# Kernel tuning notes

Measured on AMD Instinct MI355X. Metric: run time of the kernel, lower is better.

Reference implementation:

```python
import jax, jax.numpy as jnp
import numpy as np

NUM_CLASSES = 21
THRESH = 0.5
NEGPOS = 3
VAR0, VAR1 = 0.1, 0.2
FEAT = 19
N_ANCH = 9
B = 256
NUM_OBJS = 12
P = FEAT * FEAT * N_ANCH  # 3249


def make_priors():
    # 19x19 grid, 3 scales x 3 aspect ratios (1, 2, 1/2) -> 9 anchors/cell, center form
    cxy = (np.arange(FEAT, dtype=np.float32) + 0.5) / FEAT
    cx, cy = np.meshgrid(cxy, cxy, indexing='ij')  # [19,19]
    scales = np.array([0.1, 0.2, 0.35], dtype=np.float32)
    ratios = np.array([1.0, 2.0, 0.5], dtype=np.float32)
    w = (scales[:, None] * np.sqrt(ratios)[None, :]).reshape(-1)  # [9]
    h = (scales[:, None] / np.sqrt(ratios)[None, :]).reshape(-1)
    cx = np.broadcast_to(cx[:, :, None], (FEAT, FEAT, N_ANCH))
    cy = np.broadcast_to(cy[:, :, None], (FEAT, FEAT, N_ANCH))
    w = np.broadcast_to(w[None, None, :], (FEAT, FEAT, N_ANCH))
    h = np.broadcast_to(h[None, None, :], (FEAT, FEAT, N_ANCH))
    pri = np.stack([cx, cy, w, h], axis=-1).reshape(-1, 4)
    return jnp.asarray(np.clip(pri, 1e-3, 1.0))


def setup_inputs() -> dict:
    key = jax.random.key(0)
    k1, k2, k3, k4, k5 = jax.random.split(key, 5)
    loc_data = jax.random.normal(k1, (B, P, 4), dtype=jnp.float32)
    conf_data = jax.random.normal(k2, (B, P, NUM_CLASSES), dtype=jnp.float32)
    priors = make_priors()
    xy = jax.random.uniform(k3, (B, NUM_OBJS, 2), minval=0.05, maxval=0.65)
    wh = jax.random.uniform(k4, (B, NUM_OBJS, 2), minval=0.05, maxval=0.30)
    labels = jax.random.randint(k5, (B, NUM_OBJS), 0, NUM_CLASSES - 1).astype(jnp.float32)
    targets = jnp.concatenate([xy, xy + wh, labels[..., None]], axis=-1)  # [B,O,5]
    return {"loc_data": loc_data, "conf_data": conf_data, "priors": priors, "targets": targets}


def point_form(boxes):  # (cx,cy,w,h) -> (x1,y1,x2,y2)
    return jnp.concatenate([boxes[:, :2] - boxes[:, 2:] / 2,
                            boxes[:, :2] + boxes[:, 2:] / 2], axis=1)


def jaccard(a, b):  # a: [n,4], b: [m,4] point form -> [n,m]
    lt = jnp.maximum(a[:, None, :2], b[None, :, :2])
    rb = jnp.minimum(a[:, None, 2:], b[None, :, 2:])
    inter = jnp.prod(jnp.clip(rb - lt, 0.0, None), axis=-1)
    area_a = jnp.prod(a[:, 2:] - a[:, :2], axis=-1)
    area_b = jnp.prod(b[:, 2:] - b[:, :2], axis=-1)
    return inter / (area_a[:, None] + area_b[None, :] - inter)


def encode(matched, priors):  # matched point-form [P,4], priors center-form [P,4]
    g_cxcy = ((matched[:, :2] + matched[:, 2:]) / 2 - priors[:, :2]) / (VAR0 * priors[:, 2:])
    g_wh = jnp.log((matched[:, 2:] - matched[:, :2]) / priors[:, 2:]) / VAR1
    return jnp.concatenate([g_cxcy, g_wh], axis=1)


def match_one(truths, labels, priors, priors_pt):
    overlaps = jaccard(truths, priors_pt)          # [O,P]
    best_prior_idx = jnp.argmax(overlaps, axis=1)  # [O]
    best_truth_ov = jnp.max(overlaps, axis=0)      # [P]
    best_truth_idx = jnp.argmax(overlaps, axis=0)  # [P]
    best_truth_ov = best_truth_ov.at[best_prior_idx].set(2.0)
    best_truth_idx = best_truth_idx.at[best_prior_idx].set(jnp.arange(truths.shape[0]))
    matches = truths[best_truth_idx]               # [P,4]
    conf = labels[best_truth_idx] + 1
    conf = jnp.where(best_truth_ov < THRESH, 0, conf)
    return encode(matches, priors), conf


def reference(loc_data, conf_data, priors, targets):
    truths = targets[:, :, :4]
    labels = targets[:, :, 4].astype(jnp.int32)
    priors_pt = point_form(priors)
    loc_t, conf_t = jax.vmap(lambda t, l: match_one(t, l, priors, priors_pt))(truths, labels)
    loc_t = jax.lax.stop_gradient(loc_t)
    conf_t = jax.lax.stop_gradient(conf_t)

    pos = conf_t > 0                                               # [B,P]
    # smooth L1 (sum) over matched priors
    d = loc_data - loc_t
    ad = jnp.abs(d)
    sl1 = jnp.where(ad < 1.0, 0.5 * d * d, ad - 0.5)
    loss_l = jnp.sum(sl1 * pos[..., None].astype(sl1.dtype))

    # per-prior CE = logsumexp - logit[target]
    lse = jax.nn.logsumexp(conf_data, axis=-1)                     # [B,P]
    gathered = jnp.take_along_axis(conf_data, conf_t[..., None], axis=2)[..., 0]
    ce = lse - gathered                                            # [B,P]

    # hard negative mining: double argsort rank of neg losses
    loss_c_mine = jnp.where(pos, 0.0, ce)
    loss_idx = jnp.argsort(-loss_c_mine, axis=1)
    idx_rank = jnp.argsort(loss_idx, axis=1)
    num_pos = jnp.sum(pos, axis=1, keepdims=True)                  # [B,1]
    num_neg = jnp.minimum(NEGPOS * num_pos, P - 1)
    neg = idx_rank < num_neg

    sel = pos | neg
    loss_c = jnp.sum(jnp.where(sel, ce, 0.0))

    have_centerloss = jnp.max(sel.reshape(B, FEAT, FEAT, N_ANCH), axis=3).reshape(-1)
    conf_t_featuremap = jnp.max(conf_t.reshape(B, FEAT, FEAT, N_ANCH), axis=3).reshape(-1)

    N = jnp.sum(num_pos).astype(loc_data.dtype)
    return loss_l / N, loss_c / N, conf_t_featuremap, have_centerloss
```

## Files before the change

### kernel.cpp

```cpp
#include <hip/hip_runtime.h>
#include <math.h>

#pragma clang fp contract(off)

#define BB      256
#define PP      3249
#define NCLS    21
#define NOBJ    12
#define CELLS   361
#define THRESH_ 0.5f


__global__ __launch_bounds__(1024) void match_kernel(
    const float* __restrict__ loc,
    const float* __restrict__ priors, const float* __restrict__ targets,
    int* __restrict__ conf_t,
    int* __restrict__ numpos, double* __restrict__ lossl)
{
    const int b = blockIdx.x, tid = threadIdx.x;
    const int lane = tid & 63, wid = tid >> 6;
    __shared__ float s_tx1[NOBJ], s_ty1[NOBJ], s_tx2[NOBJ], s_ty2[NOBJ];
    __shared__ float s_area_t[NOBJ];
    __shared__ int   s_label[NOBJ];
    __shared__ float s_bov[PP];
    __shared__ short s_bidx[PP];
    __shared__ int   s_bpi[NOBJ];
    __shared__ float s_wov[NOBJ][16];
    __shared__ int   s_widx[NOBJ][16];
    __shared__ double s_pl[16];
    __shared__ int    s_pn[16];

    if (tid < NOBJ) {
        const float* t = targets + ((size_t)b * NOBJ + tid) * 5;
        float x1 = t[0], y1 = t[1], x2 = t[2], y2 = t[3];
        s_tx1[tid] = x1; s_ty1[tid] = y1; s_tx2[tid] = x2; s_ty2[tid] = y2;
        s_label[tid] = (int)t[4];
        s_area_t[tid] = (x2 - x1) * (y2 - y1);
    }
    __syncthreads();

    float l_bov[NOBJ];
    int   l_bidx[NOBJ];
#pragma unroll
    for (int j = 0; j < NOBJ; ++j) { l_bov[j] = -1.0f; l_bidx[j] = 0x7FFFFFFF; }

    for (int p = tid; p < PP; p += 1024) {
        float cx = priors[4*p+0], cy = priors[4*p+1], w = priors[4*p+2], h = priors[4*p+3];
        float px1 = cx - w / 2.0f, py1 = cy - h / 2.0f;
        float px2 = cx + w / 2.0f, py2 = cy + h / 2.0f;
        float area_p = (px2 - px1) * (py2 - py1);
        float bov = -1.0f; int bidx = 0;
#pragma unroll
        for (int j = 0; j < NOBJ; ++j) {
            float ltx = fmaxf(s_tx1[j], px1);
            float lty = fmaxf(s_ty1[j], py1);
            float rbx = fminf(s_tx2[j], px2);
            float rby = fminf(s_ty2[j], py2);
            float iw = fmaxf(rbx - ltx, 0.0f);
            float ih = fmaxf(rby - lty, 0.0f);
            float inter = iw * ih;
            float iou = inter / ((s_area_t[j] + area_p) - inter);
            if (iou > bov) { bov = iou; bidx = j; }
            if (iou > l_bov[j]) { l_bov[j] = iou; l_bidx[j] = p; }
        }
        s_bov[p] = bov;
        s_bidx[p] = (short)bidx;
    }

#pragma unroll
    for (int j = 0; j < NOBJ; ++j) {
        float ov = l_bov[j]; int ix = l_bidx[j];
#pragma unroll
        for (int off = 32; off > 0; off >>= 1) {
            float ov2 = __shfl_xor(ov, off);
            int   ix2 = __shfl_xor(ix, off);
            if (ov2 > ov || (ov2 == ov && ix2 < ix)) { ov = ov2; ix = ix2; }
        }
        if (lane == 0) { s_wov[j][wid] = ov; s_widx[j][wid] = ix; }
    }
    __syncthreads();

    if (tid < NOBJ) {
        float ov = s_wov[tid][0]; int ix = s_widx[tid][0];
#pragma unroll
        for (int w2 = 1; w2 < 16; ++w2) {
            float ov2 = s_wov[tid][w2]; int ix2 = s_widx[tid][w2];
            if (ov2 > ov || (ov2 == ov && ix2 < ix)) { ov = ov2; ix = ix2; }
        }
        s_bpi[tid] = ix;
    }
    __syncthreads();

    int my_pos = 0;
    double my_lossl = 0.0;
    for (int p = tid; p < PP; p += 1024) {
        int jov = -1;
#pragma unroll
        for (int j = 0; j < NOBJ; ++j) if (s_bpi[j] == p) jov = j;
        int idx; float ov;
        if (jov >= 0) { idx = jov; ov = 2.0f; }
        else          { idx = (int)s_bidx[p]; ov = s_bov[p]; }
        int c = (ov < THRESH_) ? 0 : (s_label[idx] + 1);
        conf_t[(size_t)b * PP + p] = c;

        if (c > 0) {
            ++my_pos;
            float cx = priors[4*p+0], cy = priors[4*p+1], w = priors[4*p+2], h = priors[4*p+3];
            float m0 = s_tx1[idx], m1 = s_ty1[idx], m2 = s_tx2[idx], m3 = s_ty2[idx];
            float g0 = ((m0 + m2) / 2.0f - cx) / (0.1f * w);
            float g1 = ((m1 + m3) / 2.0f - cy) / (0.1f * h);
            float g2 = logf((m2 - m0) / w) / 0.2f;
            float g3 = logf((m3 - m1) / h) / 0.2f;
            const float* ld = loc + ((size_t)b * PP + p) * 4;
            float d0 = ld[0] - g0, d1 = ld[1] - g1, d2 = ld[2] - g2, d3 = ld[3] - g3;
            float a0 = fabsf(d0), a1 = fabsf(d1), a2 = fabsf(d2), a3 = fabsf(d3);
            my_lossl += (double)((a0 < 1.0f) ? 0.5f * d0 * d0 : a0 - 0.5f);
            my_lossl += (double)((a1 < 1.0f) ? 0.5f * d1 * d1 : a1 - 0.5f);
            my_lossl += (double)((a2 < 1.0f) ? 0.5f * d2 * d2 : a2 - 0.5f);
            my_lossl += (double)((a3 < 1.0f) ? 0.5f * d3 * d3 : a3 - 0.5f);
        }
    }
#pragma unroll
    for (int off = 32; off > 0; off >>= 1) {
        my_lossl += __shfl_down(my_lossl, off);
        my_pos   += __shfl_down(my_pos, off);
    }
    if (lane == 0) { s_pl[wid] = my_lossl; s_pn[wid] = my_pos; }
    __syncthreads();
    if (tid == 0) {
        double L = 0.0; int n = 0;
#pragma unroll
        for (int w2 = 0; w2 < 16; ++w2) { L += s_pl[w2]; n += s_pn[w2]; }
        lossl[b] = L; numpos[b] = n;
    }
}

__global__ __launch_bounds__(256) void ce_kernel(
    const float* __restrict__ conf, const int* __restrict__ conf_t,
    float* __restrict__ ce_out)
{
    __shared__ float s_row[256 * NCLS];
    const int tid = threadIdx.x;
    const size_t base = (size_t)blockIdx.x * 256;
    const float4* src = (const float4*)(conf + base * NCLS);
    float4* dst = (float4*)s_row;
#pragma unroll
    for (int i = tid; i < 1344; i += 256) dst[i] = src[i];
    __syncthreads();

    const float* cd = s_row + tid * NCLS;
    float m = cd[0];
#pragma unroll
    for (int k = 1; k < NCLS; ++k) m = fmaxf(m, cd[k]);
    float s = 0.0f;
#pragma unroll
    for (int k = 0; k < NCLS; ++k) s += expf(cd[k] - m);
    float lse = logf(s) + m;
    const size_t r = base + tid;
    int c = conf_t[r];
    ce_out[r] = lse - cd[c];
}

__global__ __launch_bounds__(1024) void mine_kernel(
    const int* __restrict__ conf_t, const float* __restrict__ ce,
    const int* __restrict__ numpos, double* __restrict__ lossc,
    float* __restrict__ out)
{
    const int b = blockIdx.x, tid = threadIdx.x;
    const int lane = tid & 63, wid = tid >> 6;
    __shared__ unsigned long long s_key[PP];
    __shared__ unsigned char s_ct[PP];
    __shared__ unsigned char s_sel[PP];
    __shared__ int s_hist[256];
    __shared__ int s_chosen, s_knext;
    __shared__ double s_part[16];

    const int np = numpos[b];
    const int nneg = min(3 * np, PP - 1);

    for (int i = tid; i < PP; i += 1024) {
        int c = conf_t[(size_t)b * PP + i];
        float v = (c > 0) ? 0.0f : ce[(size_t)b * PP + i];
        s_key[i] = ((unsigned long long)__float_as_uint(v) << 32)
                 | (unsigned int)(0xFFFFFFFFu - (unsigned int)i);
        s_ct[i] = (unsigned char)c;
    }
    __syncthreads();

    unsigned long long prefix = 0ull, pmask = 0ull;
    int kk = nneg;
    for (int d = 56; d >= 0; d -= 8) {
        if (tid < 256) s_hist[tid] = 0;
        __syncthreads();
        for (int i = tid; i < PP; i += 1024) {
            unsigned long long key = s_key[i];
            if ((key & pmask) == prefix)
                atomicAdd(&s_hist[(int)((key >> d) & 0xFF)], 1);
        }
        __syncthreads();
        if (tid < 64) {
            int h0 = s_hist[4*lane+0], h1 = s_hist[4*lane+1];
            int h2 = s_hist[4*lane+2], h3 = s_hist[4*lane+3];
            int ls = h0 + h1 + h2 + h3;
            int x = ls;
#pragma unroll
            for (int off = 1; off < 64; off <<= 1) {
                int y = __shfl_down(x, off);
                if (lane + off < 64) x += y;
            }
            int excl = x - ls;
            int cb3 = excl;
            int cb2 = cb3 + h3;
            int cb1 = cb2 + h2;
            int cb0 = cb1 + h1;
            if (cb3 < kk && kk <= cb3 + h3) { s_chosen = 4*lane+3; s_knext = kk - cb3; }
            if (cb2 < kk && kk <= cb2 + h2) { s_chosen = 4*lane+2; s_knext = kk - cb2; }
            if (cb1 < kk && kk <= cb1 + h1) { s_chosen = 4*lane+1; s_knext = kk - cb1; }
            if (cb0 < kk && kk <= cb0 + h0) { s_chosen = 4*lane+0; s_knext = kk - cb0; }
        }
        __syncthreads();
        prefix |= ((unsigned long long)(unsigned int)s_chosen) << d;
        pmask  |= 0xFFull << d;
        kk = s_knext;
        __syncthreads();
    }
    const unsigned long long kth = prefix;

    double my_c = 0.0;
    for (int p = tid; p < PP; p += 1024) {
        int c = s_ct[p];
        unsigned long long key = s_key[p];
        bool sel = (c > 0) || (key >= kth);
        s_sel[p] = sel ? 1 : 0;
        if (sel) {
            if (c > 0) my_c += (double)ce[(size_t)b * PP + p];
            else       my_c += (double)__uint_as_float((unsigned int)(key >> 32));
        }
    }
    __syncthreads();

    for (int cI = tid; cI < CELLS; cI += 1024) {
        int mc = 0, hv = 0;
#pragma unroll
        for (int a = 0; a < 9; ++a) {
            int p = cI * 9 + a;
            int cv = s_ct[p];
            mc = (cv > mc) ? cv : mc;
            hv |= s_sel[p];
        }
        out[2 + (size_t)b * CELLS + cI] = (float)mc;
        out[2 + (size_t)BB * CELLS + (size_t)b * CELLS + cI] = (float)hv;
    }

#pragma unroll
    for (int off = 32; off > 0; off >>= 1) my_c += __shfl_down(my_c, off);
    if (lane == 0) s_part[wid] = my_c;
    __syncthreads();
    if (tid == 0) {
        double L = 0.0;
#pragma unroll
        for (int w2 = 0; w2 < 16; ++w2) L += s_part[w2];
        lossc[b] = L;
    }
}

__global__ __launch_bounds__(256) void finalize_kernel(
    const int* __restrict__ numpos, const double* __restrict__ lossl,
    const double* __restrict__ lossc, float* __restrict__ out)
{
    __shared__ double s_l[256], s_c[256];
    __shared__ int s_n[256];
    int tid = threadIdx.x;
    s_n[tid] = numpos[tid];
    s_l[tid] = lossl[tid];
    s_c[tid] = lossc[tid];
    __syncthreads();
    for (int s = 128; s > 0; s >>= 1) {
        if (tid < s) { s_n[tid] += s_n[tid + s]; s_l[tid] += s_l[tid + s]; s_c[tid] += s_c[tid + s]; }
        __syncthreads();
    }
    if (tid == 0) {
        double N = (double)s_n[0];
        out[0] = (float)(s_l[0] / N);
        out[1] = (float)(s_c[0] / N);
    }
}

extern "C" void kernel_launch(void* const* d_in, const int* in_sizes, int n_in,
                              void* d_out, int out_size, void* d_ws, size_t ws_size,
                              hipStream_t stream) {
    const float* loc     = (const float*)d_in[0];
    const float* conf    = (const float*)d_in[1];
    const float* priors  = (const float*)d_in[2];
    const float* targets = (const float*)d_in[3];
    float* out = (float*)d_out;

    double* ws_lossl = (double*)d_ws;
    double* ws_lossc = ws_lossl + BB;
    int*    ws_numpos = (int*)(ws_lossc + BB);
    int*    ws_conf   = ws_numpos + BB;
    float*  ws_ce     = (float*)(ws_conf + (size_t)BB * PP);

    hipLaunchKernelGGL(match_kernel, dim3(BB), dim3(1024), 0, stream,
                       loc, priors, targets, ws_conf, ws_numpos, ws_lossl);
    hipLaunchKernelGGL(ce_kernel, dim3(PP), dim3(256), 0, stream,
                       conf, ws_conf, ws_ce);
    hipLaunchKernelGGL(mine_kernel, dim3(BB), dim3(1024), 0, stream,
                       ws_conf, ws_ce, ws_numpos, ws_lossc, out);
    hipLaunchKernelGGL(finalize_kernel, dim3(1), dim3(256), 0, stream,
                       ws_numpos, ws_lossl, ws_lossc, out);
}
```

Measured before the change: 149.2 us.

## Fuse matching, cross-entropy and hard-negative mining into one per-image kernel

Merges the match, CE and mining kernels into a single kernel with one block per image. Conf_t, CE and the sort keys now stay in shared memory, which removes the global round trips through workspace and two launches. In exchange, the CE computation reads 21 strided floats per thread straight from global memory instead of staging coalesced float4 loads. It also limits the CE work to 256 blocks of 1024 threads rather than spreading it over 3249 blocks, and it raises shared memory use per block.

```diff
diff --git a/kernel.cpp b/kernel.cpp
--- a/kernel.cpp
+++ b/kernel.cpp
@@ -11,14 +11,15 @@
 #define THRESH_ 0.5f
 
 
-__global__ __launch_bounds__(1024) void match_kernel(
-    const float* __restrict__ loc,
+__global__ __launch_bounds__(1024) void fused_kernel(
+    const float* __restrict__ loc, const float* __restrict__ conf,
     const float* __restrict__ priors, const float* __restrict__ targets,
-    int* __restrict__ conf_t,
-    int* __restrict__ numpos, double* __restrict__ lossl)
+    int* __restrict__ numpos, double* __restrict__ lossl,
+    double* __restrict__ lossc, float* __restrict__ out)
 {
     const int b = blockIdx.x, tid = threadIdx.x;
     const int lane = tid & 63, wid = tid >> 6;
+
     __shared__ float s_tx1[NOBJ], s_ty1[NOBJ], s_tx2[NOBJ], s_ty2[NOBJ];
     __shared__ float s_area_t[NOBJ];
     __shared__ int   s_label[NOBJ];
@@ -27,8 +28,14 @@
     __shared__ int   s_bpi[NOBJ];
     __shared__ float s_wov[NOBJ][16];
     __shared__ int   s_widx[NOBJ][16];
+    __shared__ unsigned long long s_key[PP];
+    __shared__ unsigned char s_ct[PP];
+    __shared__ unsigned char s_sel[PP];
+    __shared__ int s_hist[256];
+    __shared__ int s_chosen, s_knext, s_nneg;
     __shared__ double s_pl[16];
     __shared__ int    s_pn[16];
+    __shared__ double s_pc[16];
 
     if (tid < NOBJ) {
         const float* t = targets + ((size_t)b * NOBJ + tid) * 5;
@@ -79,7 +86,6 @@
         if (lane == 0) { s_wov[j][wid] = ov; s_widx[j][wid] = ix; }
     }
     __syncthreads();
-
     if (tid < NOBJ) {
         float ov = s_wov[tid][0]; int ix = s_widx[tid][0];
 #pragma unroll
@@ -93,6 +99,7 @@
 
     int my_pos = 0;
     double my_lossl = 0.0;
+    const float* confb = conf + (size_t)b * PP * NCLS;
     for (int p = tid; p < PP; p += 1024) {
         int jov = -1;
 #pragma unroll
@@ -101,7 +108,21 @@
         if (jov >= 0) { idx = jov; ov = 2.0f; }
         else          { idx = (int)s_bidx[p]; ov = s_bov[p]; }
         int c = (ov < THRESH_) ? 0 : (s_label[idx] + 1);
-        conf_t[(size_t)b * PP + p] = c;
+        s_ct[p] = (unsigned char)c;
+
+        const float* cd = confb + (size_t)p * NCLS;
+        float m = cd[0];
+#pragma unroll
+        for (int k = 1; k < NCLS; ++k) m = fmaxf(m, cd[k]);
+        float s = 0.0f;
+#pragma unroll
+        for (int k = 0; k < NCLS; ++k) s += expf(cd[k] - m);
+        float ce = (logf(s) + m) - cd[c];
+
+        float v = (c > 0) ? 0.0f : ce;
+        s_key[p] = ((unsigned long long)__float_as_uint(v) << 32)
+                 | (unsigned int)(0xFFFFFFFFu - (unsigned int)p);
+        s_bov[p] = ce;
 
         if (c > 0) {
             ++my_pos;
@@ -132,63 +153,12 @@
 #pragma unroll
         for (int w2 = 0; w2 < 16; ++w2) { L += s_pl[w2]; n += s_pn[w2]; }
         lossl[b] = L; numpos[b] = n;
-    }
-}
-
-__global__ __launch_bounds__(256) void ce_kernel(
-    const float* __restrict__ conf, const int* __restrict__ conf_t,
-    float* __restrict__ ce_out)
-{
-    __shared__ float s_row[256 * NCLS];
-    const int tid = threadIdx.x;
-    const size_t base = (size_t)blockIdx.x * 256;
-    const float4* src = (const float4*)(conf + base * NCLS);
-    float4* dst = (float4*)s_row;
-#pragma unroll
-    for (int i = tid; i < 1344; i += 256) dst[i] = src[i];
-    __syncthreads();
-
-    const float* cd = s_row + tid * NCLS;
-    float m = cd[0];
-#pragma unroll
-    for (int k = 1; k < NCLS; ++k) m = fmaxf(m, cd[k]);
-    float s = 0.0f;
-#pragma unroll
-    for (int k = 0; k < NCLS; ++k) s += expf(cd[k] - m);
-    float lse = logf(s) + m;
-    const size_t r = base + tid;
-    int c = conf_t[r];
-    ce_out[r] = lse - cd[c];
-}
-
-__global__ __launch_bounds__(1024) void mine_kernel(
-    const int* __restrict__ conf_t, const float* __restrict__ ce,
-    const int* __restrict__ numpos, double* __restrict__ lossc,
-    float* __restrict__ out)
-{
-    const int b = blockIdx.x, tid = threadIdx.x;
-    const int lane = tid & 63, wid = tid >> 6;
-    __shared__ unsigned long long s_key[PP];
-    __shared__ unsigned char s_ct[PP];
-    __shared__ unsigned char s_sel[PP];
-    __shared__ int s_hist[256];
-    __shared__ int s_chosen, s_knext;
-    __shared__ double s_part[16];
-
-    const int np = numpos[b];
-    const int nneg = min(3 * np, PP - 1);
-
-    for (int i = tid; i < PP; i += 1024) {
-        int c = conf_t[(size_t)b * PP + i];
-        float v = (c > 0) ? 0.0f : ce[(size_t)b * PP + i];
-        s_key[i] = ((unsigned long long)__float_as_uint(v) << 32)
-                 | (unsigned int)(0xFFFFFFFFu - (unsigned int)i);
-        s_ct[i] = (unsigned char)c;
+        s_nneg = min(3 * n, PP - 1);
     }
     __syncthreads();
 
     unsigned long long prefix = 0ull, pmask = 0ull;
-    int kk = nneg;
+    int kk = s_nneg;
     for (int d = 56; d >= 0; d -= 8) {
         if (tid < 256) s_hist[tid] = 0;
         __syncthreads();
@@ -229,13 +199,9 @@
     double my_c = 0.0;
     for (int p = tid; p < PP; p += 1024) {
         int c = s_ct[p];
-        unsigned long long key = s_key[p];
-        bool sel = (c > 0) || (key >= kth);
+        bool sel = (c > 0) || (s_key[p] >= kth);
         s_sel[p] = sel ? 1 : 0;
-        if (sel) {
-            if (c > 0) my_c += (double)ce[(size_t)b * PP + p];
-            else       my_c += (double)__uint_as_float((unsigned int)(key >> 32));
-        }
+        if (sel) my_c += (double)s_bov[p];
     }
     __syncthreads();
 
@@ -254,12 +220,12 @@
 
 #pragma unroll
     for (int off = 32; off > 0; off >>= 1) my_c += __shfl_down(my_c, off);
-    if (lane == 0) s_part[wid] = my_c;
+    if (lane == 0) s_pc[wid] = my_c;
     __syncthreads();
     if (tid == 0) {
         double L = 0.0;
 #pragma unroll
-        for (int w2 = 0; w2 < 16; ++w2) L += s_part[w2];
+        for (int w2 = 0; w2 < 16; ++w2) L += s_pc[w2];
         lossc[b] = L;
     }
 }
@@ -295,18 +261,12 @@
     const float* targets = (const float*)d_in[3];
     float* out = (float*)d_out;
 
-    double* ws_lossl = (double*)d_ws;
-    double* ws_lossc = ws_lossl + BB;
+    double* ws_lossl  = (double*)d_ws;
+    double* ws_lossc  = ws_lossl + BB;
     int*    ws_numpos = (int*)(ws_lossc + BB);
-    int*    ws_conf   = ws_numpos + BB;
-    float*  ws_ce     = (float*)(ws_conf + (size_t)BB * PP);
-
-    hipLaunchKernelGGL(match_kernel, dim3(BB), dim3(1024), 0, stream,
-                       loc, priors, targets, ws_conf, ws_numpos, ws_lossl);
-    hipLaunchKernelGGL(ce_kernel, dim3(PP), dim3(256), 0, stream,
-                       conf, ws_conf, ws_ce);
-    hipLaunchKernelGGL(mine_kernel, dim3(BB), dim3(1024), 0, stream,
-                       ws_conf, ws_ce, ws_numpos, ws_lossc, out);
+
+    hipLaunchKernelGGL(fused_kernel, dim3(BB), dim3(1024), 0, stream,
+                       loc, conf, priors, targets, ws_numpos, ws_lossl, ws_lossc, out);
     hipLaunchKernelGGL(finalize_kernel, dim3(1), dim3(256), 0, stream,
                        ws_numpos, ws_lossl, ws_lossc, out);
 }
```

Result: faster. 141.1 us (-5.4%).
